# Kernel tuning notes

Measured on AMD Instinct MI355X. Metric: run time of the kernel, lower is better.

The kernel has to match this reference:

```python
import jax, jax.numpy as jnp
import numpy as np
from jax import lax

SCORE_THRESHOLD = 0.01
NMS_THRESHOLD = 0.5
MAX_DETECTIONS = 100
PRE_NMS_TOPK = 512  # fixed-shape candidate pool per class (tf NMS is unbounded; 512 >> max_detections covers it)
NEG_INF = -jnp.inf


def setup_inputs() -> dict:
    key = jax.random.key(0)
    k1, k2, k3, k4, k5 = jax.random.split(key, 5)
    B, N, C = 32, 50000, 10
    # valid (x1,y1,x2,y2) boxes: random top-left + positive width/height
    xy = jax.random.uniform(k1, (B, N, 2), dtype=jnp.float32) * 500.0
    wh = jax.random.uniform(k2, (B, N, 2), dtype=jnp.float32) * 100.0 + 1.0
    boxes = jnp.concatenate([xy, xy + wh], axis=-1)
    classification = jax.random.uniform(k3, (B, N, C), dtype=jnp.float32)
    rotation = jax.random.normal(k4, (B, N, 3), dtype=jnp.float32)
    translation = jax.random.normal(k5, (B, N, 3), dtype=jnp.float32)
    return {"boxes": boxes, "classification": classification,
            "rotation": rotation, "translation": translation}


def _iou_matrix(b):  # b: (K,4) in (x1,y1,x2,y2)
    x1, y1, x2, y2 = b[:, 0], b[:, 1], b[:, 2], b[:, 3]
    area = (x2 - x1) * (y2 - y1)  # (K,)
    ix1 = jnp.maximum(x1[:, None], x1[None, :])
    iy1 = jnp.maximum(y1[:, None], y1[None, :])
    ix2 = jnp.minimum(x2[:, None], x2[None, :])
    iy2 = jnp.minimum(y2[:, None], y2[None, :])
    inter = jnp.maximum(ix2 - ix1, 0.0) * jnp.maximum(iy2 - iy1, 0.0)
    union = area[:, None] + area[None, :] - inter
    return jnp.where(union > 0.0, inter / union, 0.0)  # (K,K)


def _greedy_nms_keep(iou, valid):
    # iou: (K,K) for boxes already sorted by descending score; valid: (K,) bool
    K = iou.shape[0]
    def body(suppressed, xs):
        iou_row, valid_i, i = xs
        keep_i = valid_i & jnp.logical_not(suppressed[i])
        suppressed = jnp.where(keep_i, suppressed | (iou_row > NMS_THRESHOLD), suppressed)
        return suppressed, keep_i
    _, keep = lax.scan(body, jnp.zeros((K,), bool), (iou, valid, jnp.arange(K)))
    return keep


def _per_class(scores, boxes_i):
    # scores: (N,), boxes_i: (N,4) -> kept candidate scores (K,) (-inf where dropped) and anchor idx (K,)
    sc = jnp.where(scores > SCORE_THRESHOLD, scores, NEG_INF)
    vals, idx = lax.top_k(sc, PRE_NMS_TOPK)          # sorted desc
    valid = vals > SCORE_THRESHOLD                    # also false for -inf pads
    iou = _iou_matrix(boxes_i[idx])
    keep = _greedy_nms_keep(iou, valid)
    keep = keep & (jnp.cumsum(keep.astype(jnp.int32)) <= MAX_DETECTIONS)
    return jnp.where(keep, vals, NEG_INF), idx


def _per_image(boxes_i, cls_i, rot_i, trans_i):
    # boxes_i (N,4), cls_i (N,C), rot_i (N,3), trans_i (N,3)
    C = cls_i.shape[1]
    sc_ck, idx_ck = jax.vmap(_per_class, in_axes=(1, None))(cls_i, boxes_i)  # (C,K)
    labels_ck = jnp.broadcast_to(jnp.arange(C, dtype=jnp.int32)[:, None], sc_ck.shape)
    sc_flat = sc_ck.reshape(-1)
    idx_flat = idx_ck.reshape(-1)
    lab_flat = labels_ck.reshape(-1)
    top_scores, sel = lax.top_k(sc_flat, MAX_DETECTIONS)   # global top-k across classes
    sel_idx = idx_flat[sel]
    sel_lab = lab_flat[sel]
    valid = jnp.isfinite(top_scores)
    out_boxes = jnp.where(valid[:, None], boxes_i[sel_idx], -1.0)
    out_scores = jnp.where(valid, top_scores, -1.0)
    out_labels = jnp.where(valid, sel_lab, -1).astype(jnp.int32)
    out_rot = jnp.where(valid[:, None], rot_i[sel_idx], -1.0)
    out_trans = jnp.where(valid[:, None], trans_i[sel_idx], -1.0)
    return out_boxes, out_scores, out_labels, out_rot, out_trans


def reference(boxes, classification, rotation, translation):
    return jax.vmap(_per_image)(boxes, classification, rotation, translation)
```

## Files before the change

kernel.cpp:

```cpp
#include <hip/hip_runtime.h>
#include <math.h>

typedef unsigned int u32;
typedef unsigned long long u64;

constexpr int NB   = 32;
constexpr int NN   = 50000;
constexpr int NC   = 10;
constexpr int KK   = 512;
constexpr int MAXD = 100;
constexpr int CAP  = 2048;
constexpr int LCAP = 192;
constexpr int GCH  = 2500;
constexpr int KMAX = 1024;
constexpr u32 TBIN = 252;
constexpr int RLIM = 192;

constexpr int OFF_BOX = 0;
constexpr int OFF_SC  = NB * MAXD * 4;
constexpr int OFF_LB  = OFF_SC + NB * MAXD;
constexpr int OFF_RT  = OFF_LB + NB * MAXD;
constexpr int OFF_TR  = OFF_RT + NB * MAXD * 3;

__device__ __forceinline__ u32 ord_f32(float s) {
  u32 u = __float_as_uint(s);
  return (u & 0x80000000u) ? ~u : (u | 0x80000000u);
}
__device__ __forceinline__ float unord_f32(u32 o) {
  u32 u = (o & 0x80000000u) ? (o & 0x7FFFFFFFu) : ~o;
  return __uint_as_float(u);
}
__device__ __forceinline__ u64 make_key(float s, u32 i) {
  float sp = (s > 0.01f) ? s : -INFINITY;
  return ((u64)ord_f32(sp) << 32) | (u64)(u32)(~i);
}
__device__ __forceinline__ u32 digest16(float x) {
  if (!(x > 0.01f)) return 0;
  u32 q = (u32)(x * 65536.0f);
  return q > 65535u ? 65535u : q;
}
__device__ __forceinline__ float readlane_f(float v, int lane) {
  return __int_as_float(__builtin_amdgcn_readlane(__float_as_int(v), lane));
}
__device__ __forceinline__ u64 readlane_u64(u64 v, int lane) {
  u32 lo = __builtin_amdgcn_readlane((u32)v, lane);
  u32 hi = __builtin_amdgcn_readlane((u32)(v >> 32), lane);
  return ((u64)hi << 32) | lo;
}
__device__ __forceinline__ int clamp_idx(int idx) {
  return idx < 0 ? 0 : (idx >= NN ? NN - 1 : idx);
}

__global__ __launch_bounds__(512) void gather_kernel(
    const float* __restrict__ cls, u64* __restrict__ glist,
    u32* __restrict__ gcnt) {
  const int blk = blockIdx.x;
  const int b = blk / 20, ch = blk % 20;
  const float* src = cls + (size_t)b * NN * NC + (size_t)ch * GCH * NC;
  __shared__ u32 lcnt[NC];
  __shared__ u32 lbase[NC];
  __shared__ u64 lbuf[NC][LCAP];
  const int t = threadIdx.x;
  if (t < NC) lcnt[t] = 0;
  __syncthreads();
  for (int q = t; q < GCH * NC / 4; q += 512) {
    float4 v = ((const float4*)src)[q];
    float arr[4] = {v.x, v.y, v.z, v.w};
#pragma unroll
    for (int k = 0; k < 4; ++k) {
      int e = q * 4 + k;
      int c = e % 10;
      float x = arr[k];
      if ((digest16(x) >> 8) >= TBIN) {
        u32 idx = (u32)((ch * (GCH * NC) + e) / 10);
        u32 p = atomicAdd(&lcnt[c], 1u);
        if (p < (u32)LCAP) {
          lbuf[c][p] = make_key(x, idx);
        } else {
          u32 g = atomicAdd(&gcnt[b * NC + c], 1u);
          if (g < (u32)CAP) glist[(size_t)(b * NC + c) * CAP + g] = make_key(x, idx);
        }
      }
    }
  }
  __syncthreads();
  if (t < NC) {
    u32 n = min(lcnt[t], (u32)LCAP);
    lbase[t] = atomicAdd(&gcnt[b * NC + t], n);
  }
  __syncthreads();
  for (int c = 0; c < NC; ++c) {
    u32 n = min(lcnt[c], (u32)LCAP);
    u32 base = lbase[c];
    for (u32 i = t; i < n; i += 512) {
      u32 p = base + i;
      if (p < (u32)CAP) glist[(size_t)(b * NC + c) * CAP + p] = lbuf[c][i];
    }
  }
}

__global__ __launch_bounds__(512) void selnms_kernel(
    const float* __restrict__ cls, const u64* __restrict__ glist,
    const u32* __restrict__ gcnt, const float* __restrict__ boxes,
    int* __restrict__ tidx, float* __restrict__ ksc) {
  __shared__ __align__(16) unsigned char smem[28736];
  u64* cand = (u64*)smem;
  ushort (*prank)[8] = (ushort(*)[8])(smem + 8192);
  u64* sel = (u64*)(smem + 24576);
  u64* kmask = (u64*)(smem + 28672);
  u64 (*rowm)[8] = (u64(*)[8])smem;
  float4* bx4 = (float4*)(smem + 12288);
  float* ars = (float*)(smem + 20480);
  __shared__ int s_cnt, s_d;

  const int bc = blockIdx.x;
  const int b = bc / NC;
  const int t = threadIdx.x;
  const int lane = t & 63, wv = t >> 6;

  int M = (int)gcnt[bc];
  if (M >= KK && M <= KMAX) {
    for (int i = t; i < KMAX; i += 512)
      cand[i] = (i < M) ? glist[(size_t)bc * CAP + i] : (u64)i;
  } else {
    const int c = bc % NC;
    const float* sbase = cls + (size_t)b * NN * NC + c;
    u32* hist = (u32*)prank;
    for (int i = t; i < 4096; i += 512) hist[i] = 0;
    if (t == 0) s_cnt = 0;
    __syncthreads();
    for (int i = t; i < NN; i += 512)
      atomicAdd(&hist[digest16(sbase[(size_t)i * NC]) >> 4], 1u);
    __syncthreads();
    if (t == 0) {
      u32 run = 0, d = 1;
      for (int i = 4095; i >= 1; --i) {
        run += hist[i];
        if (run >= (u32)KK) { d = (u32)i; break; }
        d = 1;
      }
      s_d = (int)d;
    }
    __syncthreads();
    const u32 dstar = (u32)s_d;
    for (int i = t; i < KMAX; i += 512) cand[i] = (u64)i;
    __syncthreads();
    for (int i = t; i < NN; i += 512) {
      float x = sbase[(size_t)i * NC];
      u32 dg = digest16(x) >> 4;
      if (dg >= dstar && dg >= 1) {
        int p = atomicAdd(&s_cnt, 1);
        if (p < KMAX) cand[p] = make_key(x, (u32)i);
      }
    }
    __syncthreads();
    M = min(s_cnt, KMAX);
  }
  sel[t] = make_key(-INFINITY, 0);
  __syncthreads();

  {
    u64 myk[16];
#pragma unroll
    for (int k = 0; k < 16; ++k) myk[k] = cand[lane + k * 64];
    int rnk[16];
#pragma unroll
    for (int k = 0; k < 16; ++k) rnk[k] = 0;
    const int j0 = wv * 128;
    const int rem = M - j0;
    const int jjmax = rem <= 0 ? 0 : (rem >= 128 ? 64 : ((rem + 1) >> 1));
    for (int jj = 0; jj < jjmax; ++jj) {
      const ulonglong2 v = *(const ulonglong2*)&cand[j0 + jj * 2];
#pragma unroll
      for (int k = 0; k < 16; ++k) {
        rnk[k] += (v.x > myk[k]) ? 1 : 0;
        rnk[k] += (v.y > myk[k]) ? 1 : 0;
      }
    }
#pragma unroll
    for (int k = 0; k < 16; ++k) prank[lane + k * 64][wv] = (ushort)rnk[k];
  }
  __syncthreads();
#pragma unroll
  for (int h = 0; h < 2; ++h) {
    const int i = h * 512 + t;
    const uint4 pv = *(const uint4*)&prank[i][0];
    const int r = (int)(pv.x & 0xFFFFu) + (int)(pv.x >> 16) +
                  (int)(pv.y & 0xFFFFu) + (int)(pv.y >> 16) +
                  (int)(pv.z & 0xFFFFu) + (int)(pv.z >> 16) +
                  (int)(pv.w & 0xFFFFu) + (int)(pv.w >> 16);
    if (i < M && r < KK) sel[r] = cand[i];
  }
  __syncthreads();

  {
    const u64 k = sel[t];
    const int idx = clamp_idx((int)(~(u32)k));
    tidx[bc * KK + t] = idx;
    const float4 bx = *(const float4*)(boxes + ((size_t)b * NN + idx) * 4);
    bx4[t] = bx;
    ars[t] = (bx.z - bx.x) * (bx.w - bx.y);
  }
  __syncthreads();

  float jx1[8], jy1[8], jx2[8], jy2[8], jar[8];
#pragma unroll
  for (int q = 0; q < 8; ++q) {
    const float4 bb = bx4[q * 64 + lane];
    jx1[q] = bb.x; jy1[q] = bb.y; jx2[q] = bb.z; jy2[q] = bb.w;
    jar[q] = ars[q * 64 + lane];
  }
  __syncthreads();


#pragma unroll
  for (int g = 0; g < RLIM / 64; ++g) {
    for (int rr = 0; rr < 8; ++rr) {
      const int il = wv + 8 * rr;
      const int i = g * 64 + il;
      const float bix1 = readlane_f(jx1[g], il);
      const float biy1 = readlane_f(jy1[g], il);
      const float bix2 = readlane_f(jx2[g], il);
      const float biy2 = readlane_f(jy2[g], il);
      const float bia  = readlane_f(jar[g], il);
      u64 m[8];
#pragma unroll
      for (int q = 0; q < 8; ++q) {
        m[q] = 0;
        if (q >= g) {
          float ix1 = fmaxf(bix1, jx1[q]);
          float iy1 = fmaxf(biy1, jy1[q]);
          float ix2 = fminf(bix2, jx2[q]);
          float iy2 = fminf(biy2, jy2[q]);
          float iw = fmaxf(ix2 - ix1, 0.0f);
          float ih = fmaxf(iy2 - iy1, 0.0f);
          float inter = iw * ih;
          float uni = bia + jar[q] - inter;
          bool s = (uni > 0.0f) && ((inter - 0.5f * uni) > uni * 0x1p-25f);
          m[q] = __ballot(s);
        }
      }
      u64 word = m[0];
#pragma unroll
      for (int q = 1; q < 8; ++q) word = (lane == q) ? m[q] : word;
      if (lane < 8) rowm[i][lane] = word;
    }
  }
  __syncthreads();

  if (wv == 0) {
    u64 vw_[8], kw[8];
#pragma unroll
    for (int q = 0; q < 8; ++q) {
      const float sc = unord_f32((u32)(sel[q * 64 + lane] >> 32));
      vw_[q] = __ballot(sc > 0.01f);
      kw[q] = 0;
    }
    u64 vsup = 0;
    int count = 0;
    bool done = false;
#pragma unroll
    for (int w = 0; w < 8; ++w) {
      if (!done) {
        u64 av = vw_[w] & ~readlane_u64(vsup, w);
        while (av) {
          const int bbit = (int)__builtin_ctzll(av);
          const int i = w * 64 + bbit;
          kw[w] |= 1ull << bbit;
          if (++count == MAXD) { done = true; break; }
          if (w < RLIM / 64) {
            const u64 row = (lane < 8) ? rowm[i][lane] : 0;
            vsup |= row;
          } else {
            const float bix1 = readlane_f(jx1[w], bbit);
            const float biy1 = readlane_f(jy1[w], bbit);
            const float bix2 = readlane_f(jx2[w], bbit);
            const float biy2 = readlane_f(jy2[w], bbit);
            const float bia  = readlane_f(jar[w], bbit);
            u64 m[8];
#pragma unroll
            for (int q = 0; q < 8; ++q) {
              m[q] = 0;
              if (q >= w) {
                float ix1 = fmaxf(bix1, jx1[q]);
                float iy1 = fmaxf(biy1, jy1[q]);
                float ix2 = fminf(bix2, jx2[q]);
                float iy2 = fminf(biy2, jy2[q]);
                float iw = fmaxf(ix2 - ix1, 0.0f);
                float ih = fmaxf(iy2 - iy1, 0.0f);
                float inter = iw * ih;
                float uni = bia + jar[q] - inter;
                bool s = (uni > 0.0f) && ((inter - 0.5f * uni) > uni * 0x1p-25f);
                m[q] = __ballot(s);
              }
            }
            u64 word = m[0];
#pragma unroll
            for (int q = 1; q < 8; ++q) word = (lane == q) ? m[q] : word;
            vsup |= word;
          }
          const u64 mask_gt = (bbit == 63) ? 0ull : (~0ull << (bbit + 1));
          av = vw_[w] & ~readlane_u64(vsup, w) & mask_gt;
        }
      }
    }
    if (lane < 8) {
      u64 word = kw[0];
#pragma unroll
      for (int q = 1; q < 8; ++q) word = (lane == q) ? kw[q] : word;
      kmask[lane] = word;
    }
  }
  __syncthreads();
  {
    const float sc = unord_f32((u32)(sel[t] >> 32));
    const bool keep = (kmask[t >> 6] >> (t & 63)) & 1ull;
    ksc[(size_t)bc * KK + t] = keep ? sc : -INFINITY;
  }
}

__global__ __launch_bounds__(512) void final_kernel(
    const float* __restrict__ boxes, const float* __restrict__ rot,
    const float* __restrict__ trans, const int* __restrict__ tidx,
    const float* __restrict__ ksc, float* __restrict__ out) {
  const int b = blockIdx.x;
  __shared__ __align__(16) u64 ck[KMAX];
  __shared__ __align__(16) ushort prank[KMAX][8];
  __shared__ u64 top[MAXD];
  __shared__ int cnt;
  const int t = threadIdx.x;
  const int lane = t & 63, wv = t >> 6;
  if (t == 0) cnt = 0;
  if (t < MAXD) top[t] = make_key(-INFINITY, 0);
  for (int i = t; i < KMAX; i += 512) ck[i] = (u64)i;
  __syncthreads();
  for (int j = t; j < NC * KK; j += 512) {
    float s = ksc[b * NC * KK + j];
    if (s != -INFINITY) {
      int p = atomicAdd(&cnt, 1);
      if (p < KMAX) ck[p] = ((u64)ord_f32(s) << 32) | (u64)(u32)(~(u32)j);
    }
  }
  __syncthreads();
  const int n = min(cnt, KMAX);
  {
    u64 myk[16];
#pragma unroll
    for (int k = 0; k < 16; ++k) myk[k] = ck[lane + k * 64];
    int rnk[16];
#pragma unroll
    for (int k = 0; k < 16; ++k) rnk[k] = 0;
    const int j0 = wv * 128;
    const int rem = n - j0;
    const int jjmax = rem <= 0 ? 0 : (rem >= 128 ? 64 : ((rem + 1) >> 1));
    for (int jj = 0; jj < jjmax; ++jj) {
      const ulonglong2 v = *(const ulonglong2*)&ck[j0 + jj * 2];
#pragma unroll
      for (int k = 0; k < 16; ++k) {
        rnk[k] += (v.x > myk[k]) ? 1 : 0;
        rnk[k] += (v.y > myk[k]) ? 1 : 0;
      }
    }
#pragma unroll
    for (int k = 0; k < 16; ++k) prank[lane + k * 64][wv] = (ushort)rnk[k];
  }
  __syncthreads();
#pragma unroll
  for (int h = 0; h < 2; ++h) {
    const int i = h * 512 + t;
    const uint4 pv = *(const uint4*)&prank[i][0];
    const int r = (int)(pv.x & 0xFFFFu) + (int)(pv.x >> 16) +
                  (int)(pv.y & 0xFFFFu) + (int)(pv.y >> 16) +
                  (int)(pv.z & 0xFFFFu) + (int)(pv.z >> 16) +
                  (int)(pv.w & 0xFFFFu) + (int)(pv.w >> 16);
    if (i < n && r < MAXD) top[r] = ck[i];
  }
  __syncthreads();

  if (t < MAXD) {
    float b0 = -1.f, b1 = -1.f, b2 = -1.f, b3 = -1.f;
    float os = -1.f, ol = -1.f;
    float r0 = -1.f, r1 = -1.f, r2 = -1.f;
    float t0 = -1.f, t1 = -1.f, t2 = -1.f;
    const u64 k = top[t];
    const float sc = unord_f32((u32)(k >> 32));
    if (sc != -INFINITY) {
      int j = (int)(~(u32)k);
      int c = j >> 9, slot = j & (KK - 1);
      int idx = tidx[(b * NC + c) * KK + slot];
      os = sc;
      ol = (float)c;
      const float4 bx = *(const float4*)(boxes + ((size_t)b * NN + idx) * 4);
      b0 = bx.x; b1 = bx.y; b2 = bx.z; b3 = bx.w;
      const float* rp = rot + ((size_t)b * NN + idx) * 3;
      r0 = rp[0]; r1 = rp[1]; r2 = rp[2];
      const float* tp = trans + ((size_t)b * NN + idx) * 3;
      t0 = tp[0]; t1 = tp[1]; t2 = tp[2];
    }
    const int o = b * MAXD + t;
    out[OFF_BOX + (size_t)o * 4 + 0] = b0;
    out[OFF_BOX + (size_t)o * 4 + 1] = b1;
    out[OFF_BOX + (size_t)o * 4 + 2] = b2;
    out[OFF_BOX + (size_t)o * 4 + 3] = b3;
    out[OFF_SC + o] = os;
    out[OFF_LB + o] = ol;
    out[OFF_RT + (size_t)o * 3 + 0] = r0;
    out[OFF_RT + (size_t)o * 3 + 1] = r1;
    out[OFF_RT + (size_t)o * 3 + 2] = r2;
    out[OFF_TR + (size_t)o * 3 + 0] = t0;
    out[OFF_TR + (size_t)o * 3 + 1] = t1;
    out[OFF_TR + (size_t)o * 3 + 2] = t2;
  }
}

extern "C" void kernel_launch(void* const* d_in, const int* in_sizes, int n_in,
                              void* d_out, int out_size, void* d_ws, size_t ws_size,
                              hipStream_t stream) {
  const float* boxes = (const float*)d_in[0];
  const float* cls   = (const float*)d_in[1];
  const float* rot   = (const float*)d_in[2];
  const float* trans = (const float*)d_in[3];
  float* out = (float*)d_out;

  u64* glist = (u64*)d_ws;
  int* tidx  = (int*)(glist + (size_t)NB * NC * CAP);
  float* ksc = (float*)(tidx + NB * NC * KK);
  u32* gcnt  = (u32*)(ksc + NB * NC * KK);

  hipMemsetAsync(gcnt, 0, NB * NC * sizeof(u32), stream);
  gather_kernel<<<NB * 20, 512, 0, stream>>>(cls, glist, gcnt);
  selnms_kernel<<<NB * NC, 512, 0, stream>>>(cls, glist, gcnt, boxes, tidx, ksc);
  final_kernel<<<NB, 512, 0, stream>>>(boxes, rot, trans, tidx, ksc, out);
}
```

Before: 115.6 us.

## Split select+NMS into a two-block-per-class sort kernel and a separate NMS kernel

The fused select/NMS kernel becomes two kernels. A rank-sort kernel launches two blocks per (image, class), each ranking half of the candidates, and writes the sorted keys and gathered boxes to global workspace. In that kernel the box loads for the fast path are issued before the ranking loop so their latency overlaps it. A separate NMS kernel reads the presorted keys and boxes, which doubles parallelism in the sort stage and cuts per-thread register use. Both kernels also remap block order across images. The cost is an extra kernel launch, the fallback path being computed redundantly by both blocks, and a global round trip for the intermediate keys and boxes.

```diff
diff --git a/kernel.cpp b/kernel.cpp
--- a/kernel.cpp
+++ b/kernel.cpp
@@ -99,33 +99,28 @@
   }
 }
 
-__global__ __launch_bounds__(512) void selnms_kernel(
+__global__ __launch_bounds__(512) void sort_kernel(
     const float* __restrict__ cls, const u64* __restrict__ glist,
     const u32* __restrict__ gcnt, const float* __restrict__ boxes,
-    int* __restrict__ tidx, float* __restrict__ ksc) {
-  __shared__ __align__(16) unsigned char smem[28736];
+    u64* __restrict__ selg, float4* __restrict__ bxg) {
+  __shared__ __align__(16) unsigned char smem[16448];
   u64* cand = (u64*)smem;
   ushort (*prank)[8] = (ushort(*)[8])(smem + 8192);
-  u64* sel = (u64*)(smem + 24576);
-  u64* kmask = (u64*)(smem + 28672);
-  u64 (*rowm)[8] = (u64(*)[8])smem;
-  float4* bx4 = (float4*)(smem + 12288);
-  float* ars = (float*)(smem + 20480);
   __shared__ int s_cnt, s_d;
-
-  const int bc = blockIdx.x;
+  const int p = blockIdx.x >> 1, half = blockIdx.x & 1;
+  const int bc = (p & 7) * 40 + (p >> 3);
   const int b = bc / NC;
-  const int t = threadIdx.x;
-  const int lane = t & 63, wv = t >> 6;
+  const int t = threadIdx.x, lane = t & 63, wv = t >> 6;
 
   int M = (int)gcnt[bc];
-  if (M >= KK && M <= KMAX) {
+  const bool fast = (M >= KK && M <= KMAX);
+  if (fast) {
     for (int i = t; i < KMAX; i += 512)
       cand[i] = (i < M) ? glist[(size_t)bc * CAP + i] : (u64)i;
   } else {
     const int c = bc % NC;
     const float* sbase = cls + (size_t)b * NN * NC + c;
-    u32* hist = (u32*)prank;
+    u32* hist = (u32*)smem;
     for (int i = t; i < 4096; i += 512) hist[i] = 0;
     if (t == 0) s_cnt = 0;
     __syncthreads();
@@ -149,57 +144,97 @@
       float x = sbase[(size_t)i * NC];
       u32 dg = digest16(x) >> 4;
       if (dg >= dstar && dg >= 1) {
-        int p = atomicAdd(&s_cnt, 1);
-        if (p < KMAX) cand[p] = make_key(x, (u32)i);
+        int pq = atomicAdd(&s_cnt, 1);
+        if (pq < KMAX) cand[pq] = make_key(x, (u32)i);
       }
     }
     __syncthreads();
     M = min(s_cnt, KMAX);
   }
-  sel[t] = make_key(-INFINITY, 0);
-  __syncthreads();
+
+  u64 ck0 = 0;
+  float4 pb0;
+  if (fast) {
+    ck0 = cand[half * 512 + t];
+    const int pidx = clamp_idx((int)(~(u32)ck0));
+    pb0 = *(const float4*)(boxes + ((size_t)b * NN + pidx) * 4);
+  }
+  __syncthreads();
+
+  const int h2lo = fast ? half : 0;
+  const int h2hi = fast ? half : 1;
+  for (int h2 = h2lo; h2 <= h2hi; ++h2) {
+    {
+      u64 myk[8];
+#pragma unroll
+      for (int k = 0; k < 8; ++k) myk[k] = cand[h2 * 512 + lane + k * 64];
+      int rnk[8];
+#pragma unroll
+      for (int k = 0; k < 8; ++k) rnk[k] = 0;
+      const int j0 = wv * 128;
+      const int rem = M - j0;
+      const int jjmax = rem <= 0 ? 0 : (rem >= 128 ? 64 : ((rem + 1) >> 1));
+      for (int jj = 0; jj < jjmax; ++jj) {
+        const ulonglong2 v = *(const ulonglong2*)&cand[j0 + jj * 2];
+#pragma unroll
+        for (int k = 0; k < 8; ++k) {
+          rnk[k] += (v.x > myk[k]) ? 1 : 0;
+          rnk[k] += (v.y > myk[k]) ? 1 : 0;
+        }
+      }
+#pragma unroll
+      for (int k = 0; k < 8; ++k) prank[lane + k * 64][wv] = (ushort)rnk[k];
+    }
+    __syncthreads();
+    {
+      const uint4 pv = *(const uint4*)&prank[t][0];
+      const int r = (int)(pv.x & 0xFFFFu) + (int)(pv.x >> 16) +
+                    (int)(pv.y & 0xFFFFu) + (int)(pv.y >> 16) +
+                    (int)(pv.z & 0xFFFFu) + (int)(pv.z >> 16) +
+                    (int)(pv.w & 0xFFFFu) + (int)(pv.w >> 16);
+      const int ig = h2 * 512 + t;
+      if (ig < M && r < KK) {
+        const u64 key = fast ? ck0 : cand[ig];
+        selg[(size_t)bc * KK + r] = key;
+        if (fast) {
+          bxg[(size_t)bc * KK + r] = pb0;
+        } else {
+          const int pidx = clamp_idx((int)(~(u32)key));
+          bxg[(size_t)bc * KK + r] =
+              *(const float4*)(boxes + ((size_t)b * NN + pidx) * 4);
+        }
+      }
+    }
+    if (h2 < h2hi) __syncthreads();
+  }
+  if (M < KK) {
+    for (int r = M + t; r < KK; r += 512) {
+      selg[(size_t)bc * KK + r] = make_key(-INFINITY, 0);
+      bxg[(size_t)bc * KK + r] =
+          *(const float4*)(boxes + ((size_t)b * NN + 0) * 4);
+    }
+  }
+}
+
+__global__ __launch_bounds__(512) void nms_kernel(
+    const u64* __restrict__ selg, const float4* __restrict__ bxg,
+    int* __restrict__ tidx, float* __restrict__ ksc) {
+  __shared__ __align__(16) unsigned char smem[26560];
+  float4* bx4 = (float4*)smem;
+  float* ars = (float*)(smem + 8192);
+  float* sscore = (float*)(smem + 10240);
+  u64 (*rowm)[9] = (u64(*)[9])(smem + 12288);
+  u64* kmask = (u64*)(smem + 26432);
+  const int bc = (blockIdx.x & 7) * 40 + (blockIdx.x >> 3);
+  const int t = threadIdx.x, lane = t & 63, wv = t >> 6;
 
   {
-    u64 myk[16];
-#pragma unroll
-    for (int k = 0; k < 16; ++k) myk[k] = cand[lane + k * 64];
-    int rnk[16];
-#pragma unroll
-    for (int k = 0; k < 16; ++k) rnk[k] = 0;
-    const int j0 = wv * 128;
-    const int rem = M - j0;
-    const int jjmax = rem <= 0 ? 0 : (rem >= 128 ? 64 : ((rem + 1) >> 1));
-    for (int jj = 0; jj < jjmax; ++jj) {
-      const ulonglong2 v = *(const ulonglong2*)&cand[j0 + jj * 2];
-#pragma unroll
-      for (int k = 0; k < 16; ++k) {
-        rnk[k] += (v.x > myk[k]) ? 1 : 0;
-        rnk[k] += (v.y > myk[k]) ? 1 : 0;
-      }
-    }
-#pragma unroll
-    for (int k = 0; k < 16; ++k) prank[lane + k * 64][wv] = (ushort)rnk[k];
-  }
-  __syncthreads();
-#pragma unroll
-  for (int h = 0; h < 2; ++h) {
-    const int i = h * 512 + t;
-    const uint4 pv = *(const uint4*)&prank[i][0];
-    const int r = (int)(pv.x & 0xFFFFu) + (int)(pv.x >> 16) +
-                  (int)(pv.y & 0xFFFFu) + (int)(pv.y >> 16) +
-                  (int)(pv.z & 0xFFFFu) + (int)(pv.z >> 16) +
-                  (int)(pv.w & 0xFFFFu) + (int)(pv.w >> 16);
-    if (i < M && r < KK) sel[r] = cand[i];
-  }
-  __syncthreads();
-
-  {
-    const u64 k = sel[t];
-    const int idx = clamp_idx((int)(~(u32)k));
-    tidx[bc * KK + t] = idx;
-    const float4 bx = *(const float4*)(boxes + ((size_t)b * NN + idx) * 4);
+    const u64 k = selg[(size_t)bc * KK + t];
+    tidx[bc * KK + t] = clamp_idx((int)(~(u32)k));
+    const float4 bx = bxg[(size_t)bc * KK + t];
     bx4[t] = bx;
     ars[t] = (bx.z - bx.x) * (bx.w - bx.y);
+    sscore[t] = unord_f32((u32)(k >> 32));
   }
   __syncthreads();
 
@@ -210,7 +245,6 @@
     jx1[q] = bb.x; jy1[q] = bb.y; jx2[q] = bb.z; jy2[q] = bb.w;
     jar[q] = ars[q * 64 + lane];
   }
-  __syncthreads();
 
 
 #pragma unroll
@@ -252,7 +286,7 @@
     u64 vw_[8], kw[8];
 #pragma unroll
     for (int q = 0; q < 8; ++q) {
-      const float sc = unord_f32((u32)(sel[q * 64 + lane] >> 32));
+      const float sc = sscore[q * 64 + lane];
       vw_[q] = __ballot(sc > 0.01f);
       kw[q] = 0;
     }
@@ -313,7 +347,7 @@
   }
   __syncthreads();
   {
-    const float sc = unord_f32((u32)(sel[t] >> 32));
+    const float sc = sscore[t];
     const bool keep = (kmask[t >> 6] >> (t & 63)) & 1ull;
     ksc[(size_t)bc * KK + t] = keep ? sc : -INFINITY;
   }
@@ -422,13 +456,16 @@
   const float* trans = (const float*)d_in[3];
   float* out = (float*)d_out;
 
-  u64* glist = (u64*)d_ws;
-  int* tidx  = (int*)(glist + (size_t)NB * NC * CAP);
-  float* ksc = (float*)(tidx + NB * NC * KK);
-  u32* gcnt  = (u32*)(ksc + NB * NC * KK);
+  u64* glist   = (u64*)d_ws;
+  u64* selg    = glist + (size_t)NB * NC * CAP;
+  float4* bxg  = (float4*)(selg + (size_t)NB * NC * KK);
+  int* tidx    = (int*)(bxg + (size_t)NB * NC * KK);
+  float* ksc   = (float*)(tidx + NB * NC * KK);
+  u32* gcnt    = (u32*)(ksc + NB * NC * KK);
 
   hipMemsetAsync(gcnt, 0, NB * NC * sizeof(u32), stream);
   gather_kernel<<<NB * 20, 512, 0, stream>>>(cls, glist, gcnt);
-  selnms_kernel<<<NB * NC, 512, 0, stream>>>(cls, glist, gcnt, boxes, tidx, ksc);
+  sort_kernel<<<NB * NC * 2, 512, 0, stream>>>(cls, glist, gcnt, boxes, selg, bxg);
+  nms_kernel<<<NB * NC, 512, 0, stream>>>(selg, bxg, tidx, ksc);
   final_kernel<<<NB, 512, 0, stream>>>(boxes, rot, trans, tidx, ksc, out);
 }
```

Measured after the change: 111.0 us. -4.0%, faster.
